# Kernel optimization log

Measured on AMD Instinct MI355X. Metric: run time of the kernel, lower is better.

The kernel has to match this reference:

```python
import jax, jax.numpy as jnp
import numpy as np

B, T, V, E, H, L = 32, 128, 32000, 1024, 1024, 3


def lstm_layer(x, Wx, Wh, b, h0, c0):
    """Standard LSTM (i,f,g,o gate order). x: [B,T,D]. Returns ([B,T,H], (h,c))."""
    def step(carry, xt):
        h, c = carry
        z = xt @ Wx + h @ Wh + b          # [B, 4H]
        i, f, g, o = jnp.split(z, 4, axis=-1)
        c = jax.nn.sigmoid(f) * c + jax.nn.sigmoid(i) * jnp.tanh(g)
        h = jax.nn.sigmoid(o) * jnp.tanh(c)
        return (h, c), h
    (h, c), ys = jax.lax.scan(step, (h0, c0), jnp.swapaxes(x, 0, 1))
    return jnp.swapaxes(ys, 0, 1), (h, c)


def setup_inputs() -> dict:
    key = jax.random.key(0)
    ks = jax.random.split(key, 12)
    s = 0.05  # small init to avoid gate saturation
    inp = {
        "enc_ids": jax.random.randint(ks[0], (B, T), 0, V, dtype=jnp.int32),
        "dec_ids": jax.random.randint(ks[1], (B, T), 0, V, dtype=jnp.int32),
        "emb": jax.random.normal(ks[2], (V, E), jnp.float32) * s,
        "Wx_enc": jax.random.normal(ks[3], (L, E, 4 * H), jnp.float32) * s,
        "Wh_enc": jax.random.normal(ks[4], (L, H, 4 * H), jnp.float32) * s,
        "b_enc": jnp.zeros((L, 4 * H), jnp.float32),
        "Wx_dec": jax.random.normal(ks[5], (L, E, 4 * H), jnp.float32) * s,
        "Wh_dec": jax.random.normal(ks[6], (L, H, 4 * H), jnp.float32) * s,
        "b_dec": jnp.zeros((L, 4 * H), jnp.float32),
        "dense_W": jax.random.normal(ks[7], (H, V), jnp.float32) * s,
        "dense_b": jnp.zeros((V,), jnp.float32),
    }
    return inp


def reference(enc_ids, dec_ids, emb, Wx_enc, Wh_enc, b_enc, Wx_dec, Wh_dec, b_dec, dense_W, dense_b):
    zeros = jnp.zeros((B, H), jnp.float32)
    # encoder: 3 stacked LSTMs, zero initial state each
    x = emb[enc_ids]                                      # [B,T,E]
    state = (zeros, zeros)
    for l in range(L):
        x, state = lstm_layer(x, Wx_enc[l], Wh_enc[l], b_enc[l], zeros, zeros)
    # decoder: faithful to source state chaining:
    # dec layer0 init = enc layer2 final; dec layer_{i+1} init = dec layer_i final
    y = emb[dec_ids]                                      # [B,T,E]
    for l in range(L):
        y, state = lstm_layer(y, Wx_dec[l], Wh_dec[l], b_dec[l], state[0], state[1])
    logits = y.reshape(-1, H) @ dense_W + dense_b          # [B*T, V]
    return logits.reshape(B, T, V)
```

## Files before the change

### kernel.cpp

```cpp
#include <hip/hip_runtime.h>


typedef __bf16 bf8 __attribute__((ext_vector_type(8)));
typedef float  f4  __attribute__((ext_vector_type(4)));

#define TLEN  128
#define HID   1024
#define G4    4096
#define VOC   32000
#define NBLK_SEQ 64

__device__ __forceinline__ ushort f2bf(float f) {
  unsigned u = __builtin_bit_cast(unsigned, f);
  u += 0x7fffu + ((u >> 16) & 1u);
  return (ushort)(u >> 16);
}
__device__ __forceinline__ float sigmoidf_(float x) { return 1.f / (1.f + expf(-x)); }

__device__ __forceinline__ void ld16_sys(uint4& v, const void* p) {
  asm volatile("global_load_dwordx4 %0, %1, off sc0 sc1" : "=v"(v) : "v"(p));
}
__device__ __forceinline__ unsigned ld4_sys(const void* p) {
  unsigned v;
  asm volatile("global_load_dword %0, %1, off sc0 sc1\n\ts_waitcnt vmcnt(0)"
               : "=v"(v) : "v"(p) : "memory");
  return v;
}
__device__ __forceinline__ void ld4_sys3(unsigned& a, unsigned& b, unsigned& c,
                                         const void* pa, const void* pb, const void* pc) {
  asm volatile("global_load_dword %0, %3, off sc0 sc1\n\t"
               "global_load_dword %1, %4, off sc0 sc1\n\t"
               "global_load_dword %2, %5, off sc0 sc1\n\t"
               "s_waitcnt vmcnt(0)"
               : "=&v"(a), "=&v"(b), "=&v"(c)
               : "v"(pa), "v"(pb), "v"(pc) : "memory");
}
__device__ __forceinline__ void st4_sys(void* p, unsigned v) {
  asm volatile("global_store_dword %0, %1, off sc0 sc1" :: "v"(p), "v"(v) : "memory");
}
__device__ __forceinline__ void st2_sys(void* p, unsigned v) {
  asm volatile("global_store_short %0, %1, off sc0 sc1" :: "v"(p), "v"(v) : "memory");
}
__device__ __forceinline__ void wait_vm0() {
  asm volatile("s_waitcnt vmcnt(0)" ::: "memory");
  __builtin_amdgcn_sched_barrier(0);
}

typedef const __attribute__((address_space(1))) void GvoidC;
typedef __attribute__((address_space(3))) void Lvoid;
__device__ __forceinline__ void g2l16(const void* g, void* l) {
  __builtin_amdgcn_global_load_lds((GvoidC*)g, (Lvoid*)l, 16, 0, 0);
}

__global__ __launch_bounds__(256) void embed_kernel(const int* __restrict__ ids,
    const float* __restrict__ emb, ushort* __restrict__ out) {
  int r = blockIdx.x;
  int b = r & 31, t = r >> 5;
  int id = ids[b * TLEN + t];
  const float4* src = (const float4*)(emb + (size_t)id * HID);
  float4 v = src[threadIdx.x];
  ushort4 o;
  o.x = f2bf(v.x); o.y = f2bf(v.y); o.z = f2bf(v.z); o.w = f2bf(v.w);
  *(ushort4*)(out + (size_t)r * HID + threadIdx.x * 4) = o;
}

__global__ __launch_bounds__(256) void transpose_cvt(const float* __restrict__ W,
    ushort* __restrict__ Wt, int R, int C) {
  __shared__ float tile[32][33];
  int tx = threadIdx.x & 31, ty = threadIdx.x >> 5;
  int c0 = blockIdx.x * 32, r0 = blockIdx.y * 32;
  #pragma unroll
  for (int i = 0; i < 32; i += 8)
    tile[ty + i][tx] = W[(size_t)(r0 + ty + i) * C + c0 + tx];
  __syncthreads();
  #pragma unroll
  for (int i = 0; i < 32; i += 8)
    Wt[(size_t)(c0 + ty + i) * R + r0 + tx] = f2bf(tile[tx][ty + i]);
}

__global__ __launch_bounds__(256) void gemm_bt(const ushort* __restrict__ A,
    const ushort* __restrict__ Bt, const float* __restrict__ bias,
    float* __restrict__ C, int M, int N, int K, int permute) {
  __shared__ __align__(16) ushort lA[128 * 32];
  __shared__ __align__(16) ushort lB[128 * 32];
  int tid = threadIdx.x;
  int lane = tid & 63, wave = tid >> 6;
  int m0 = blockIdx.y * 128, n0 = blockIdx.x * 128;
  int wr = wave >> 1, wc = wave & 1;
  f4 zero = {0.f, 0.f, 0.f, 0.f};
  f4 acc[4][4];
  #pragma unroll
  for (int i = 0; i < 4; i++)
    #pragma unroll
    for (int j = 0; j < 4; j++) acc[i][j] = zero;

  const ushort* Ag = A  + (size_t)(m0 + wave * 32 + (lane >> 2)) * K + (lane & 3) * 8;
  const ushort* Bg = Bt + (size_t)(n0 + wave * 32 + (lane >> 2)) * K + (lane & 3) * 8;
  ushort* lAp = lA + wave * 32 * 32;
  ushort* lBp = lB + wave * 32 * 32;

  for (int kt = 0; kt < K; kt += 32) {
    g2l16(Ag + kt, lAp);
    g2l16(Ag + (size_t)16 * K + kt, lAp + 16 * 32);
    g2l16(Bg + kt, lBp);
    g2l16(Bg + (size_t)16 * K + kt, lBp + 16 * 32);
    __syncthreads();
    bf8 aF[4], bF[4];
    #pragma unroll
    for (int i = 0; i < 4; i++)
      aF[i] = *(const bf8*)(lA + (wr * 64 + i * 16 + (lane & 15)) * 32 + (lane >> 4) * 8);
    #pragma unroll
    for (int j = 0; j < 4; j++)
      bF[j] = *(const bf8*)(lB + (wc * 64 + j * 16 + (lane & 15)) * 32 + (lane >> 4) * 8);
    #pragma unroll
    for (int i = 0; i < 4; i++)
      #pragma unroll
      for (int j = 0; j < 4; j++)
        acc[i][j] = __builtin_amdgcn_mfma_f32_16x16x32_bf16(aF[i], bF[j], acc[i][j], 0, 0, 0);
    __syncthreads();
  }
  #pragma unroll
  for (int i = 0; i < 4; i++) {
    #pragma unroll
    for (int j = 0; j < 4; j++) {
      int col = n0 + wc * 64 + j * 16 + (lane & 15);
      float bv = bias ? bias[col] : 0.f;
      #pragma unroll
      for (int v = 0; v < 4; v++) {
        int row = m0 + wr * 64 + i * 16 + (lane >> 4) * 4 + v;
        int orow = permute ? ((row & 31) * TLEN + (row >> 5)) : row;
        C[(size_t)orow * N + col] = acc[i][j][v] + bv;
      }
    }
  }
}

__global__ __launch_bounds__(512, 1) void enc_wave(
    const float*  __restrict__ Zpre,
    const ushort* __restrict__ WhT,
    const ushort* __restrict__ WxT,
    const float*  __restrict__ bE,
    ushort*       __restrict__ hxe,
    float*        __restrict__ cSe,
    ushort*       __restrict__ hS,
    unsigned*     __restrict__ flags)
{
  const int bx = blockIdx.x;
  const int l = bx >> 6, jg = bx & 63;
  const int j0 = jg * 16;
  const int tid = threadIdx.x;
  const int lane = tid & 63, wave = tid >> 6;
  const int g = wave & 3, op = wave >> 2;
  const int rr = tid >> 4, jj = tid & 15;

  __shared__ __align__(16) char hLDS[65536];
  __shared__ __align__(16) char xLDS[65536];
  __shared__ float zbuf[8][32][17];

  float cc = cSe[(size_t)l * 32768 + rr * HID + j0 + jj];
  float bias4[4];
  #pragma unroll
  for (int gg = 0; gg < 4; gg++)
    bias4[gg] = bE[l * G4 + gg * HID + j0 + jj];

  const bool mfma_on = (l > 0) || (op == 0);
  bf8 bw[32];
  if (mfma_on) {
    const ushort* Wb = op ? (WxT + (size_t)(l - 1) * G4 * HID)
                          : (WhT + (size_t)l * G4 * HID);
    const ushort* Bp = Wb + (size_t)(g * HID + j0 + (lane & 15)) * HID + (lane >> 4) * 8;
    #pragma unroll
    for (int kk = 0; kk < 32; kk++) bw[kk] = *(const bf8*)(Bp + kk * 32);
  }

  const int r0 = lane & 15, r1 = r0 + 16;
  const int klb = (lane >> 4) * 16;
  const int swz = (r0 & 7) << 4;

  float zv4[4], zn4[4];
  if (l == 0) {
    #pragma unroll
    for (int gg = 0; gg < 4; gg++)
      zv4[gg] = Zpre[(size_t)rr * G4 + gg * HID + j0 + jj];
  }

  for (int w = 0; w < 130; ++w) {
    if (w > 0) {
      if (wave == 0) {
        for (;;) {
          unsigned a, b, c;
          ld4_sys3(a, b, c, flags + lane * 4, flags + (64 + lane) * 4,
                   flags + (128 + lane) * 4);
          if (!__ballot(a < (unsigned)w || b < (unsigned)w || c < (unsigned)w)) break;
          __builtin_amdgcn_s_sleep(1);
        }
      }
      __syncthreads();
    }
    const int t = w - l;
    if (t >= 0 && t < TLEN) {
      const char* hsrc = (const char*)(hxe + ((size_t)l * 2 + ((t - 1) & 1)) * 32768);
      uint4 hreg[8], xreg[8];
      #pragma unroll
      for (int it = 0; it < 8; it++)
        ld16_sys(hreg[it], hsrc + (size_t)(tid + it * 512) * 16);
      if (l > 0) {
        const char* xsrc = (const char*)(hxe + ((size_t)(l - 1) * 2 + (t & 1)) * 32768);
        #pragma unroll
        for (int it = 0; it < 8; it++)
          ld16_sys(xreg[it], xsrc + (size_t)(tid + it * 512) * 16);
      }
      wait_vm0();
      #pragma unroll
      for (int it = 0; it < 8; it++) {
        int c = tid + it * 512;
        int row = c >> 7;
        int o = (c & 127) * 16;
        *(uint4*)(hLDS + row * 2048 + (o ^ ((row & 7) << 4))) = hreg[it];
      }
      if (l > 0) {
        #pragma unroll
        for (int it = 0; it < 8; it++) {
          int c = tid + it * 512;
          int row = c >> 7;
          int o = (c & 127) * 16;
          *(uint4*)(xLDS + row * 2048 + (o ^ ((row & 7) << 4))) = xreg[it];
        }
      }
      __syncthreads();

      if (l == 0 && t + 1 < TLEN) {
        const float* Ztn = Zpre + (size_t)(t + 1) * 32 * G4;
        #pragma unroll
        for (int gg = 0; gg < 4; gg++)
          zn4[gg] = Ztn[(size_t)rr * G4 + gg * HID + j0 + jj];
      }

      if (mfma_on) {
        const char* S = op ? xLDS : hLDS;
        f4 acc0 = {0.f, 0.f, 0.f, 0.f}, acc1 = {0.f, 0.f, 0.f, 0.f};
        #pragma unroll
        for (int kk = 0; kk < 32; kk++) {
          int cb = kk * 64 + klb;
          bf8 a0 = *(const bf8*)(S + r0 * 2048 + (cb ^ swz));
          bf8 a1 = *(const bf8*)(S + r1 * 2048 + (cb ^ swz));
          acc0 = __builtin_amdgcn_mfma_f32_16x16x32_bf16(a0, bw[kk], acc0, 0, 0, 0);
          acc1 = __builtin_amdgcn_mfma_f32_16x16x32_bf16(a1, bw[kk], acc1, 0, 0, 0);
        }
        #pragma unroll
        for (int v = 0; v < 4; v++) {
          zbuf[wave][(lane >> 4) * 4 + v][lane & 15]      = acc0[v];
          zbuf[wave][16 + (lane >> 4) * 4 + v][lane & 15] = acc1[v];
        }
      }
      __syncthreads();

      float z[4];
      #pragma unroll
      for (int gg = 0; gg < 4; gg++) z[gg] = zbuf[gg][rr][jj];
      if (l > 0) {
        #pragma unroll
        for (int gg = 0; gg < 4; gg++) z[gg] += zbuf[4 + gg][rr][jj] + bias4[gg];
      } else {
        #pragma unroll
        for (int gg = 0; gg < 4; gg++) z[gg] += zv4[gg];
        #pragma unroll
        for (int gg = 0; gg < 4; gg++) zv4[gg] = zn4[gg];
      }
      float ig = sigmoidf_(z[0]), fg = sigmoidf_(z[1]);
      float gv = tanhf(z[2]),     og = sigmoidf_(z[3]);
      cc = fg * cc + ig * gv;
      float hv = og * tanhf(cc);
      ushort hb = f2bf(hv);
      st2_sys(hxe + ((size_t)l * 2 + (t & 1)) * 32768 + rr * HID + j0 + jj, (unsigned)hb);
      if (t == TLEN - 1) {
        hS [(size_t)l * 32768 + rr * HID + j0 + jj] = hb;
        cSe[(size_t)l * 32768 + rr * HID + j0 + jj] = cc;
      }
      wait_vm0();
    }
    __syncthreads();
    if (tid == 0) st4_sys(flags + bx * 4, (unsigned)(w + 1));
  }
}

__global__ __launch_bounds__(256, 1) void lstm_seq(
    const float*  __restrict__ Zpre,
    const ushort* __restrict__ Wht,
    const ushort* __restrict__ h0,
    float*        __restrict__ cS,
    ushort*       __restrict__ yout,
    unsigned*     __restrict__ flags)
{
  const int jg = blockIdx.x;
  const int j0 = jg * 16;
  const int tid = threadIdx.x;
  const int lane = tid & 63, wave = tid >> 6;
  const int rr = tid >> 3, cp = tid & 7;

  __shared__ __align__(16) char hLDS[65536];
  __shared__ float zbuf[4][32][17];

  float2 cc = *(const float2*)(cS + (size_t)rr * HID + j0 + 2 * cp);

  const ushort* Bp = Wht + (size_t)(wave * HID + j0 + (lane & 15)) * HID + (lane >> 4) * 8;
  bf8 bw[32];
  #pragma unroll
  for (int kk = 0; kk < 32; kk++)
    bw[kk] = *(const bf8*)(Bp + kk * 32);

  const int r0 = lane & 15, r1 = r0 + 16;
  const int klb = (lane >> 4) * 16;
  const int swz = (r0 & 7) << 4;

  float2 zv[4], zn[4];
  #pragma unroll
  for (int g = 0; g < 4; g++)
    zv[g] = *(const float2*)(Zpre + (size_t)rr * G4 + g * HID + j0 + 2 * cp);

  for (int t = 0; t < TLEN; ++t) {
    if (t > 0) {
      if (wave == 0) {
        const unsigned* fp = flags + lane * 4;
        while (__ballot(ld4_sys(fp) < (unsigned)t)) __builtin_amdgcn_s_sleep(1);
      }
      __syncthreads();
    }
    const char* hsrc = (t == 0) ? (const char*)h0
                                : (const char*)(yout + (size_t)(t - 1) * 32 * HID);
    uint4 hreg[16];
    #pragma unroll
    for (int it = 0; it < 16; it++)
      ld16_sys(hreg[it], hsrc + (size_t)(tid + it * 256) * 16);
    wait_vm0();
    #pragma unroll
    for (int it = 0; it < 16; it++) {
      int c = tid + it * 256;
      int row = c >> 7;
      int o = (c & 127) * 16;
      *(uint4*)(hLDS + row * 2048 + (o ^ ((row & 7) << 4))) = hreg[it];
    }
    __syncthreads();

    if (t + 1 < TLEN) {
      const float* Ztn = Zpre + (size_t)(t + 1) * 32 * G4;
      #pragma unroll
      for (int g = 0; g < 4; g++)
        zn[g] = *(const float2*)(Ztn + (size_t)rr * G4 + g * HID + j0 + 2 * cp);
    }

    f4 acc0 = {0.f, 0.f, 0.f, 0.f}, acc1 = {0.f, 0.f, 0.f, 0.f};
    #pragma unroll
    for (int kk = 0; kk < 32; kk++) {
      int cb = kk * 64 + klb;
      bf8 a0 = *(const bf8*)(hLDS + r0 * 2048 + (cb ^ swz));
      bf8 a1 = *(const bf8*)(hLDS + r1 * 2048 + (cb ^ swz));
      acc0 = __builtin_amdgcn_mfma_f32_16x16x32_bf16(a0, bw[kk], acc0, 0, 0, 0);
      acc1 = __builtin_amdgcn_mfma_f32_16x16x32_bf16(a1, bw[kk], acc1, 0, 0, 0);
    }
    #pragma unroll
    for (int v = 0; v < 4; v++) {
      zbuf[wave][(lane >> 4) * 4 + v][lane & 15]      = acc0[v];
      zbuf[wave][16 + (lane >> 4) * 4 + v][lane & 15] = acc1[v];
    }
    __syncthreads();

    float zi0 = zv[0].x + zbuf[0][rr][2 * cp],     zi1 = zv[0].y + zbuf[0][rr][2 * cp + 1];
    float zf0 = zv[1].x + zbuf[1][rr][2 * cp],     zf1 = zv[1].y + zbuf[1][rr][2 * cp + 1];
    float zg0 = zv[2].x + zbuf[2][rr][2 * cp],     zg1 = zv[2].y + zbuf[2][rr][2 * cp + 1];
    float zo0 = zv[3].x + zbuf[3][rr][2 * cp],     zo1 = zv[3].y + zbuf[3][rr][2 * cp + 1];
    cc.x = sigmoidf_(zf0) * cc.x + sigmoidf_(zi0) * tanhf(zg0);
    cc.y = sigmoidf_(zf1) * cc.y + sigmoidf_(zi1) * tanhf(zg1);
    float hv0 = sigmoidf_(zo0) * tanhf(cc.x);
    float hv1 = sigmoidf_(zo1) * tanhf(cc.y);
    unsigned packed = (unsigned)f2bf(hv0) | ((unsigned)f2bf(hv1) << 16);
    st4_sys((char*)(yout + (size_t)t * 32 * HID) + ((size_t)rr * HID + j0 + 2 * cp) * 2,
            packed);
    #pragma unroll
    for (int g = 0; g < 4; g++) zv[g] = zn[g];

    wait_vm0();
    __syncthreads();
    if (tid == 0) st4_sys(flags + jg * 4, (unsigned)(t + 1));
  }
  *(float2*)(cS + (size_t)rr * HID + j0 + 2 * cp) = cc;
}

__global__ __launch_bounds__(256) void prep_enc(ushort* hxe, float* cSe,
                                                unsigned* flags) {
  int i = blockIdx.x * 256 + threadIdx.x;
  hxe[i] = 0;
  if (i < 98304) cSe[i] = 0.f;
  if (i < 192)   flags[i * 4] = 0;
}
__global__ __launch_bounds__(256) void prep_dec0(const ushort* __restrict__ hS2,
                                                 const float* __restrict__ cSe2,
                                                 ushort* h0, float* cS,
                                                 unsigned* flags) {
  int i = blockIdx.x * 256 + threadIdx.x;
  h0[i] = hS2[i];
  cS[i] = cSe2[i];
  if (i < NBLK_SEQ) flags[i * 4] = 0;
}
__global__ __launch_bounds__(256) void prep_copy(const ushort* __restrict__ src,
                                                 ushort* __restrict__ h0,
                                                 unsigned* __restrict__ flags) {
  int i = blockIdx.x * 256 + threadIdx.x;
  h0[i] = src[i];
  if (i < NBLK_SEQ) flags[i * 4] = 0;
}

extern "C" void kernel_launch(void* const* d_in, const int* in_sizes, int n_in,
                              void* d_out, int out_size, void* d_ws, size_t ws_size,
                              hipStream_t stream) {
  const int*   enc_ids = (const int*)d_in[0];
  const int*   dec_ids = (const int*)d_in[1];
  const float* emb     = (const float*)d_in[2];
  const float* Wx_enc  = (const float*)d_in[3];
  const float* Wh_enc  = (const float*)d_in[4];
  const float* b_enc   = (const float*)d_in[5];
  const float* Wx_dec  = (const float*)d_in[6];
  const float* Wh_dec  = (const float*)d_in[7];
  const float* b_dec   = (const float*)d_in[8];
  const float* dense_W = (const float*)d_in[9];
  const float* dense_b = (const float*)d_in[10];
  float* out = (float*)d_out;

  char* ws = (char*)d_ws;
  const size_t SZ_BUF = (size_t)4096 * 1024 * 2;
  ushort*   bufA   = (ushort*)(ws);
  ushort*   bufB   = (ushort*)(ws + SZ_BUF);
  ushort*   Wxt    = (ushort*)(ws + 2 * SZ_BUF);
  ushort*   Wht    = (ushort*)(ws + 3 * SZ_BUF);
  ushort*   dWt    = (ushort*)(ws + 4 * SZ_BUF);
  char*     p2     = ws + 4 * SZ_BUF + (size_t)VOC * 1024 * 2;
  ushort*   hstate = (ushort*)p2;
  float*    cS     = (float*)(p2 + (size_t)32 * 1024 * 2);
  unsigned* flags  = (unsigned*)(p2 + (size_t)32 * 1024 * 2 + (size_t)32 * 1024 * 4);

  char* ob = (char*)d_out;
  float*    Zpre   = out;
  ushort*   WhTe   = (ushort*)(ob + (size_t)64  * 1024 * 1024);
  ushort*   WxTe   = (ushort*)(ob + (size_t)88  * 1024 * 1024);
  char*     st     = ob + (size_t)112 * 1024 * 1024;
  ushort*   hxe    = (ushort*)st;
  float*    cSe    = (float*)(st + 393216);
  ushort*   hS     = (ushort*)(st + 786432);
  unsigned* flags2 = (unsigned*)(st + 983040);
  const size_t WSTRIDE = (size_t)G4 * HID;

  transpose_cvt<<<dim3(VOC / 32, 1024 / 32), 256, 0, stream>>>(dense_W, dWt, 1024, VOC);

  embed_kernel<<<4096, 256, 0, stream>>>(enc_ids, emb, bufA);
  transpose_cvt<<<dim3(G4 / 32, 32), 256, 0, stream>>>(Wx_enc, Wxt, 1024, G4);
  gemm_bt<<<dim3(G4 / 128, 4096 / 128), 256, 0, stream>>>(bufA, Wxt, b_enc,
                                                          Zpre, 4096, G4, 1024, 0);
  for (int l = 0; l < 3; l++)
    transpose_cvt<<<dim3(G4 / 32, 32), 256, 0, stream>>>(Wh_enc + (size_t)l * 1024 * G4,
                                                         WhTe + l * WSTRIDE, 1024, G4);
  for (int l = 1; l < 3; l++)
    transpose_cvt<<<dim3(G4 / 32, 32), 256, 0, stream>>>(Wx_enc + (size_t)l * 1024 * G4,
                                                         WxTe + (l - 1) * WSTRIDE, 1024, G4);
  prep_enc<<<768, 256, 0, stream>>>(hxe, cSe, flags2);
  enc_wave<<<192, 512, 0, stream>>>(Zpre, WhTe, WxTe, b_enc, hxe, cSe, hS, flags2);

  embed_kernel<<<4096, 256, 0, stream>>>(dec_ids, emb, bufA);
  ushort* cur = bufA; ushort* oth = bufB;
  for (int l = 0; l < 3; l++) {
    transpose_cvt<<<dim3(G4 / 32, 32), 256, 0, stream>>>(Wx_dec + (size_t)l * 1024 * G4, Wxt, 1024, G4);
    transpose_cvt<<<dim3(G4 / 32, 32), 256, 0, stream>>>(Wh_dec + (size_t)l * 1024 * G4, Wht, 1024, G4);
    gemm_bt<<<dim3(G4 / 128, 4096 / 128), 256, 0, stream>>>(cur, Wxt, b_dec + (size_t)l * G4,
                                                            Zpre, 4096, G4, 1024, 0);
    if (l == 0) {
      prep_dec0<<<128, 256, 0, stream>>>(hS + 2 * 32768, cSe + 2 * 32768, hstate, cS, flags);
    } else {
      const ushort* h0src = cur + (size_t)127 * 32 * HID;
      prep_copy<<<128, 256, 0, stream>>>(h0src, hstate, flags);
    }
    lstm_seq<<<NBLK_SEQ, 256, 0, stream>>>(Zpre, Wht, hstate, cS, oth, flags);
    ushort* tmp = cur; cur = oth; oth = tmp;
  }

  gemm_bt<<<dim3(VOC / 128, 4096 / 128), 256, 0, stream>>>(cur, dWt, dense_b, out,
                                                           4096, VOC, 1024, 1);
}
```

Measured before the change: 3.639 ms.

## Split LSTM recurrence K across waves, pack h stores, swizzle GEMM tile order

In the sequential LSTM kernel, each wave used to own one gate and walk the full K=1024. Now each wave takes a quarter of K for all four gates, giving four independent MFMA accumulation chains per row half. Partial sums are reduced through LDS, which shortens the serial MFMA dependency chain per timestep at the cost of more LDS traffic and a 4-way add. Separately, the wavefront encoder kernel packs pairs of bf16 h values with a lane shuffle into 32-bit system-coherent stores, and the GEMM remaps workgroup IDs in a stride-8 interleave to change tile placement across XCDs.

```diff
diff --git a/kernel.cpp b/kernel.cpp
--- a/kernel.cpp
+++ b/kernel.cpp
@@ -37,9 +37,6 @@
 }
 __device__ __forceinline__ void st4_sys(void* p, unsigned v) {
   asm volatile("global_store_dword %0, %1, off sc0 sc1" :: "v"(p), "v"(v) : "memory");
-}
-__device__ __forceinline__ void st2_sys(void* p, unsigned v) {
-  asm volatile("global_store_short %0, %1, off sc0 sc1" :: "v"(p), "v"(v) : "memory");
 }
 __device__ __forceinline__ void wait_vm0() {
   asm volatile("s_waitcnt vmcnt(0)" ::: "memory");
@@ -85,7 +82,11 @@
   __shared__ __align__(16) ushort lB[128 * 32];
   int tid = threadIdx.x;
   int lane = tid & 63, wave = tid >> 6;
-  int m0 = blockIdx.y * 128, n0 = blockIdx.x * 128;
+  int nwg = gridDim.x * gridDim.y;
+  int wg  = blockIdx.y * gridDim.x + blockIdx.x;
+  int q   = nwg >> 3;
+  int swg = (wg & 7) * q + (wg >> 3);
+  int m0 = (swg / gridDim.x) * 128, n0 = (swg % gridDim.x) * 128;
   int wr = wave >> 1, wc = wave & 1;
   f4 zero = {0.f, 0.f, 0.f, 0.f};
   f4 acc[4][4];
@@ -272,7 +273,11 @@
       cc = fg * cc + ig * gv;
       float hv = og * tanhf(cc);
       ushort hb = f2bf(hv);
-      st2_sys(hxe + ((size_t)l * 2 + (t & 1)) * 32768 + rr * HID + j0 + jj, (unsigned)hb);
+      unsigned u = (unsigned)hb;
+      unsigned nb = __shfl_xor(u, 1);
+      if ((jj & 1) == 0)
+        st4_sys(hxe + ((size_t)l * 2 + (t & 1)) * 32768 + rr * HID + j0 + jj,
+                u | (nb << 16));
       if (t == TLEN - 1) {
         hS [(size_t)l * 32768 + rr * HID + j0 + jj] = hb;
         cSe[(size_t)l * 32768 + rr * HID + j0 + jj] = cc;
@@ -299,19 +304,24 @@
   const int rr = tid >> 3, cp = tid & 7;
 
   __shared__ __align__(16) char hLDS[65536];
-  __shared__ float zbuf[4][32][17];
+  __shared__ float zp[4][4][32][17];
 
   float2 cc = *(const float2*)(cS + (size_t)rr * HID + j0 + 2 * cp);
 
-  const ushort* Bp = Wht + (size_t)(wave * HID + j0 + (lane & 15)) * HID + (lane >> 4) * 8;
-  bf8 bw[32];
-  #pragma unroll
-  for (int kk = 0; kk < 32; kk++)
-    bw[kk] = *(const bf8*)(Bp + kk * 32);
+  bf8 bw[4][8];
+  #pragma unroll
+  for (int g = 0; g < 4; g++) {
+    const ushort* Bp = Wht + (size_t)(g * HID + j0 + (lane & 15)) * HID
+                     + wave * 256 + (lane >> 4) * 8;
+    #pragma unroll
+    for (int kk = 0; kk < 8; kk++)
+      bw[g][kk] = *(const bf8*)(Bp + kk * 32);
+  }
 
   const int r0 = lane & 15, r1 = r0 + 16;
   const int klb = (lane >> 4) * 16;
   const int swz = (r0 & 7) << 4;
+  const int kbase = wave * 512;
 
   float2 zv[4], zn[4];
   #pragma unroll
@@ -349,30 +359,41 @@
         zn[g] = *(const float2*)(Ztn + (size_t)rr * G4 + g * HID + j0 + 2 * cp);
     }
 
-    f4 acc0 = {0.f, 0.f, 0.f, 0.f}, acc1 = {0.f, 0.f, 0.f, 0.f};
-    #pragma unroll
-    for (int kk = 0; kk < 32; kk++) {
-      int cb = kk * 64 + klb;
+    f4 acc0[4], acc1[4];
+    #pragma unroll
+    for (int g = 0; g < 4; g++) { acc0[g] = (f4){0,0,0,0}; acc1[g] = (f4){0,0,0,0}; }
+    #pragma unroll
+    for (int kk = 0; kk < 8; kk++) {
+      int cb = kbase + kk * 64 + klb;
       bf8 a0 = *(const bf8*)(hLDS + r0 * 2048 + (cb ^ swz));
       bf8 a1 = *(const bf8*)(hLDS + r1 * 2048 + (cb ^ swz));
-      acc0 = __builtin_amdgcn_mfma_f32_16x16x32_bf16(a0, bw[kk], acc0, 0, 0, 0);
-      acc1 = __builtin_amdgcn_mfma_f32_16x16x32_bf16(a1, bw[kk], acc1, 0, 0, 0);
-    }
-    #pragma unroll
-    for (int v = 0; v < 4; v++) {
-      zbuf[wave][(lane >> 4) * 4 + v][lane & 15]      = acc0[v];
-      zbuf[wave][16 + (lane >> 4) * 4 + v][lane & 15] = acc1[v];
-    }
+      #pragma unroll
+      for (int g = 0; g < 4; g++) {
+        acc0[g] = __builtin_amdgcn_mfma_f32_16x16x32_bf16(a0, bw[g][kk], acc0[g], 0, 0, 0);
+        acc1[g] = __builtin_amdgcn_mfma_f32_16x16x32_bf16(a1, bw[g][kk], acc1[g], 0, 0, 0);
+      }
+    }
+    #pragma unroll
+    for (int g = 0; g < 4; g++)
+      #pragma unroll
+      for (int v = 0; v < 4; v++) {
+        zp[wave][g][(lane >> 4) * 4 + v][lane & 15]      = acc0[g][v];
+        zp[wave][g][16 + (lane >> 4) * 4 + v][lane & 15] = acc1[g][v];
+      }
     __syncthreads();
 
-    float zi0 = zv[0].x + zbuf[0][rr][2 * cp],     zi1 = zv[0].y + zbuf[0][rr][2 * cp + 1];
-    float zf0 = zv[1].x + zbuf[1][rr][2 * cp],     zf1 = zv[1].y + zbuf[1][rr][2 * cp + 1];
-    float zg0 = zv[2].x + zbuf[2][rr][2 * cp],     zg1 = zv[2].y + zbuf[2][rr][2 * cp + 1];
-    float zo0 = zv[3].x + zbuf[3][rr][2 * cp],     zo1 = zv[3].y + zbuf[3][rr][2 * cp + 1];
-    cc.x = sigmoidf_(zf0) * cc.x + sigmoidf_(zi0) * tanhf(zg0);
-    cc.y = sigmoidf_(zf1) * cc.y + sigmoidf_(zi1) * tanhf(zg1);
-    float hv0 = sigmoidf_(zo0) * tanhf(cc.x);
-    float hv1 = sigmoidf_(zo1) * tanhf(cc.y);
+    float zx[4], zy[4];
+    #pragma unroll
+    for (int g = 0; g < 4; g++) {
+      zx[g] = zv[g].x + zp[0][g][rr][2 * cp]     + zp[1][g][rr][2 * cp]
+                      + zp[2][g][rr][2 * cp]     + zp[3][g][rr][2 * cp];
+      zy[g] = zv[g].y + zp[0][g][rr][2 * cp + 1] + zp[1][g][rr][2 * cp + 1]
+                      + zp[2][g][rr][2 * cp + 1] + zp[3][g][rr][2 * cp + 1];
+    }
+    cc.x = sigmoidf_(zx[1]) * cc.x + sigmoidf_(zx[0]) * tanhf(zx[2]);
+    cc.y = sigmoidf_(zy[1]) * cc.y + sigmoidf_(zy[0]) * tanhf(zy[2]);
+    float hv0 = sigmoidf_(zx[3]) * tanhf(cc.x);
+    float hv1 = sigmoidf_(zy[3]) * tanhf(cc.y);
     unsigned packed = (unsigned)f2bf(hv0) | ((unsigned)f2bf(hv1) << 16);
     st4_sys((char*)(yout + (size_t)t * 32 * HID) + ((size_t)rr * HID + j0 + 2 * cp) * 2,
             packed);
```

Result: no change. 3.601 ms (-1.1%).
